# Kernel optimization log

Measured on AMD Instinct MI355X. Metric: run time of the kernel, lower is better.

## Reference

```python
import jax, jax.numpy as jnp
import numpy as np
from jax import lax

N_C = 1024  # number of FPS centroids (hard-coded in forward)
K = 32      # knn neighbors (hard-coded in forward)


def _fps(x, far0):
    # Faithful to the source: dist is recomputed against ONLY the latest
    # centroid each iteration (the mask/min-update in the source is dead code),
    # then far = argmax(dist).
    B = x.shape[0]
    bidx = jnp.arange(B)

    def step(far, _):
        c = x[bidx, far]                              # [B, C]
        d = jnp.sum((x - c[:, None, :]) ** 2, -1)     # [B, N]
        return jnp.argmax(d, -1), c

    _, cents = lax.scan(step, far0, None, length=N_C)  # cents: [n_c, B, C]
    return jnp.transpose(cents, (1, 0, 2))             # [B, n_c, C]


def _knn_group(x, cent):
    # squared euclidean distances (same argsort order as torch.cdist)
    d2 = (jnp.sum(cent ** 2, -1)[..., None]
          + jnp.sum(x ** 2, -1)[:, None, :]
          - 2.0 * jnp.einsum('bmc,bnc->bmn', cent, x))   # [B, n_c, N]
    _, idx = lax.top_k(-d2, K)                            # [B, n_c, K] smallest dists
    neighbors = jax.vmap(lambda xb, ib: xb[ib])(x, idx)   # [B, n_c, K, C]
    return neighbors


def _conv1x1(h, w, b):
    # 1x1 Conv1d == channel matmul; h: [B, Cin, L], w: [Cout, Cin]
    return jax.nn.relu(jnp.einsum('oi,bil->bol', w, h) + b[None, :, None])


def setup_inputs() -> dict:
    key = jax.random.key(0)
    ks = jax.random.split(key, 20)
    B, N, C = 4, 16384, 3
    num_classes = 3
    p = lambda k, shp: (jax.random.normal(k, shp, jnp.float32) * 0.02)
    return {
        'x': jax.random.normal(ks[0], (B, N, C), jnp.float32),
        'far_init': jax.random.randint(ks[1], (B,), 0, N, jnp.int32),
        'w1': p(ks[2], (64, 3)),    'b1': p(ks[3], (64,)),
        'w2': p(ks[4], (64, 64)),   'b2': p(ks[5], (64,)),
        'w3': p(ks[6], (64, 64)),   'b3': p(ks[7], (64,)),
        'w4': p(ks[8], (128, 64)),  'b4': p(ks[9], (128,)),
        'w5': p(ks[10], (1024, 128)), 'b5': p(ks[11], (1024,)),
        'fw1': p(ks[12], (512, 1024)), 'fb1': p(ks[13], (512,)),
        'fw2': p(ks[14], (256, 512)),  'fb2': p(ks[15], (256,)),
        'fw3': p(ks[16], (num_classes, 256)), 'fb3': p(ks[17], (num_classes,)),
    }


def reference(x, far_init, w1, b1, w2, b2, w3, b3, w4, b4, w5, b5,
              fw1, fb1, fw2, fb2, fw3, fb3):
    B, N, C = x.shape
    cent = _fps(x, far_init)                 # [B, n_c, C]
    neighbors = _knn_group(x, cent)          # [B, n_c, K, C]
    h = jnp.transpose(neighbors, (0, 3, 1, 2)).reshape(B, C, N_C * K)
    h = _conv1x1(h, w1, b1)
    h = _conv1x1(h, w2, b2)
    h = _conv1x1(h, w3, b3)
    h = _conv1x1(h, w4, b4)
    h = _conv1x1(h, w5, b5)                  # [B, 1024, n_c*K]
    g = jnp.max(h, axis=2)                   # global max pool -> [B, 1024]
    g = jax.nn.relu(g @ fw1.T + fb1)
    g = jax.nn.relu(g @ fw2.T + fb2)
    return g @ fw3.T + fb3                   # [B, num_classes]
```

## Files before the change

kernel.cpp:

```cpp
#include <hip/hip_runtime.h>

#define BN  4
#define NPT 16384
#define NCC 1024
#define KNN 32

#define HBINS    2048
#define CCH      2
#define CAND_CAP 768

#define OFF_CCOUNT 0
#define OFF_SCOUNT 64
#define OFF_SBITS  128
#define OFF_POOL   (128 + BN*(NPT/32)*4)
#define OFF_CLIST  (OFF_POOL + BN*NCC*4)
#define OFF_H1     (OFF_CLIST + BN*NCC*4)
#define OFF_H2     (OFF_H1 + BN*512*4)
#define OFF_SLIST  (OFF_H2 + BN*256*4)

typedef short bf16x8 __attribute__((ext_vector_type(8)));
typedef float f32x4  __attribute__((ext_vector_type(4)));
typedef float f32x2  __attribute__((ext_vector_type(2)));

__device__ __forceinline__ short f2bf(float f) {
    unsigned u = __float_as_uint(f);
    return (short)((u + 0x7fffu + ((u >> 16) & 1u)) >> 16);
}
__device__ __forceinline__ bf16x8 cvt8(const float* __restrict__ p) {
    bf16x8 v;
#pragma unroll
    for (int j = 0; j < 8; ++j) v[j] = f2bf(p[j]);
    return v;
}

__global__ __launch_bounds__(1024) void fps_kernel(const float* __restrict__ x,
    const int* __restrict__ far_init, int* __restrict__ clist, int* __restrict__ ccount,
    int* __restrict__ scount, unsigned* __restrict__ sbits, float* __restrict__ pool)
{
#pragma clang fp contract(off)
    const int b = blockIdx.x, t = threadIdx.x;
    __shared__ __align__(16) unsigned char seen[NPT];
    __shared__ unsigned long long slot[3];

    if (t < 512) sbits[b*(NPT/32) + t] = 0u;
    pool[b*NCC + t] = 0.0f;
    if (t == 0) { ccount[b] = 0; scount[b] = 0; }

    const float* xb = x + (size_t)b * NPT * 3;
    f32x2 px[8], py[8], pz[8];
#pragma unroll
    for (int r = 0; r < 8; ++r) {
        int ia = t + ((2*r) << 10), ib = ia + 1024;
        px[r] = f32x2{xb[ia*3+0], xb[ib*3+0]};
        py[r] = f32x2{xb[ia*3+1], xb[ib*3+1]};
        pz[r] = f32x2{xb[ia*3+2], xb[ib*3+2]};
    }
    ((uint4*)seen)[t] = make_uint4(0,0,0,0);
    if (t == 0) { slot[0] = 0ull; slot[1] = 0ull; slot[2] = 0ull; }
    int prev_bx = far_init[b];
    __syncthreads();
    int pbs = __builtin_amdgcn_readfirstlane(prev_bx);
    float cx = xb[pbs*3], cy = xb[pbs*3+1], cz = xb[pbs*3+2];

    int done = 0;
    for (int it = 0; it < NCC-1; ++it) {
        const int p = it % 3;
        const f32x2 cX = {cx, cx}, cY = {cy, cy}, cZ = {cz, cz};
        float best = -1.0f; int bi = 0;
#pragma unroll
        for (int r = 0; r < 8; ++r) {
            f32x2 dx = px[r] - cX;
            f32x2 dy = py[r] - cY;
            f32x2 dz = pz[r] - cZ;
            f32x2 m1 = dx * dx;
            f32x2 m2 = dy * dy;
            f32x2 m3 = dz * dz;
            f32x2 s  = (m1 + m2) + m3;
            int ia = t + ((2*r) << 10);
            if (s.x > best) { best = s.x; bi = ia; }
            if (s.y > best) { best = s.y; bi = ia + 1024; }
        }
#pragma unroll
        for (int m = 1; m < 64; m <<= 1) {
            float od = __shfl_xor(best, m, 64);
            int   oi = __shfl_xor(bi,   m, 64);
            if (od > best || (od == best && oi < bi)) { best = od; bi = oi; }
        }
        if ((t & 63) == 0) {
            unsigned long long pk =
                (((unsigned long long)__float_as_uint(best)) << 32)
                | (unsigned)(NPT - 1 - bi);
            atomicMax(&slot[p], pk);
        }
        if (t == 0) seen[prev_bx] = 1;
        __syncthreads();
        int bx = NPT - 1 - (int)(unsigned)(slot[p] & 0xFFFFFFFFull);
        if (t == 0) slot[(it + 2) % 3] = 0ull;
        if (seen[bx]) { done = 1; break; }
        prev_bx = bx;
        int bxs = __builtin_amdgcn_readfirstlane(bx);
        cx = xb[bxs*3]; cy = xb[bxs*3+1]; cz = xb[bxs*3+2];
    }
    if (!done && t == 0) seen[prev_bx] = 1;
    __syncthreads();
#pragma unroll
    for (int j = 0; j < 16; ++j) {
        int idx = t + (j << 10);
        if (seen[idx]) {
            int pos = atomicAdd(&ccount[b], 1);
            clist[b * NCC + pos] = idx;
        }
    }
}

__device__ __forceinline__ unsigned key_of(float px, float py, float pz, float xn,
                                           float cx, float cy, float cz, float cn)
{
    float dot = __fadd_rn(__fadd_rn(__fmul_rn(cx,px), __fmul_rn(cy,py)), __fmul_rn(cz,pz));
    float d2  = __fsub_rn(__fadd_rn(cn, xn), __fmul_rn(2.0f, dot));
    unsigned u = __float_as_uint(d2);
    return u ^ ((u >> 31) ? 0xFFFFFFFFu : 0x80000000u);
}

__device__ __forceinline__ void wave_scan_bins(const unsigned* __restrict__ H,
    int nbins, int rem, int lane, int* __restrict__ out_bin, int* __restrict__ out_below)
{
    int per = nbins >> 6;
    int base = lane * per;
    unsigned part = 0;
    for (int q = 0; q < per; ++q) part += H[base + q];
    unsigned inc = part;
#pragma unroll
    for (int m = 1; m < 64; m <<= 1) {
        unsigned u = __shfl_up(inc, m, 64);
        if (lane >= m) inc += u;
    }
    unsigned exc = inc - part;
    unsigned long long mk = __ballot(exc < (unsigned)rem && inc >= (unsigned)rem);
    int src = __ffsll((long long)mk) - 1;
    if (lane == src) {
        unsigned run = exc; int bb = base;
        for (int q = 0; q < per; ++q) {
            unsigned h = H[base + q];
            if (run + h >= (unsigned)rem) { bb = base + q; break; }
            run += h;
        }
        *out_bin = bb; *out_below = (int)run;
    }
}

__global__ __launch_bounds__(1024) void knn_kernel(const float* __restrict__ x,
    const int* __restrict__ clist, const int* __restrict__ ccount,
    unsigned* __restrict__ sbits, int* __restrict__ slist, int* __restrict__ scount)
{
    const int b = blockIdx.y, t = threadIdx.x;
    const int lane = t & 63, w = t >> 6;
    const int cnt = ccount[b];
    const int cbase = blockIdx.x * CCH;
    if (cbase >= cnt) return;
    const float* xb = x + (size_t)b * NPT * 3;

    __shared__ unsigned hist[CCH * HBINS];
    __shared__ unsigned cand[CCH * CAND_CAP];
    __shared__ float cpx[CCH], cpy[CCH], cpz[CCH], cpn[CCH];
    __shared__ unsigned candCnt[CCH];
    __shared__ int s_bb[CCH], s_below[CCH], s_rrem[CCH], s_need[CCH], s_pref[CCH];
    __shared__ unsigned s_tau[CCH];
    __shared__ int s_tbin, s_tbelow;

    if (t < CCH) {
        int ci = clist[b * NCC + min(cbase + t, cnt - 1)];
        float cx = xb[ci*3], cy = xb[ci*3+1], cz = xb[ci*3+2];
        cpx[t] = cx; cpy[t] = cy; cpz[t] = cz;
        cpn[t] = __fadd_rn(__fadd_rn(__fmul_rn(cx,cx), __fmul_rn(cy,cy)), __fmul_rn(cz,cz));
        candCnt[t] = 0;
    }
    for (int i = t; i < CCH * HBINS; i += 1024) hist[i] = 0;
    __syncthreads();

    unsigned keys[NPT/1024][CCH];
#pragma unroll
    for (int j = 0; j < NPT/1024; ++j) {
        int i = t + (j << 10);
        float px = xb[i*3], py = xb[i*3+1], pz = xb[i*3+2];
        float xn = __fadd_rn(__fadd_rn(__fmul_rn(px,px), __fmul_rn(py,py)), __fmul_rn(pz,pz));
#pragma unroll
        for (int c = 0; c < CCH; ++c) {
            unsigned key = key_of(px,py,pz,xn, cpx[c],cpy[c],cpz[c],cpn[c]);
            keys[j][c] = key;
            atomicAdd(&hist[c*HBINS + (key >> 21)], 1u);
        }
    }
    __syncthreads();

    if (w < CCH)
        wave_scan_bins(&hist[w*HBINS], HBINS, KNN, lane, &s_bb[w], &s_below[w]);
    __syncthreads();
    if (t < CCH) s_rrem[t] = KNN - s_below[t];
    __syncthreads();

#pragma unroll
    for (int j = 0; j < NPT/1024; ++j) {
#pragma unroll
        for (int c = 0; c < CCH; ++c) {
            unsigned key = keys[j][c];
            if ((int)(key >> 21) == s_bb[c]) {
                unsigned pos = atomicAdd(&candCnt[c], 1u);
                if (pos < CAND_CAP) cand[c*CAND_CAP + pos] = key;
            }
        }
    }
    __syncthreads();

    if (w < CCH) {
        unsigned cc = candCnt[w];
        if (cc <= CAND_CAP) {
            int r = s_rrem[w] - 1;
            const unsigned* C = &cand[w*CAND_CAP];
            for (int idx = lane; idx < (int)cc; idx += 64) {
                unsigned k = C[idx]; int rank = 0;
                for (int q = 0; q < (int)cc; ++q) {
                    unsigned kq = C[q];
                    rank += (kq < k || (kq == k && q < idx)) ? 1 : 0;
                }
                if (rank == r) s_tau[w] = k;
            }
            if (lane == 0) s_need[w] = 0;
        } else if (lane == 0) s_need[w] = 1;
    }
    __syncthreads();

    for (int c = 0; c < CCH; ++c) {
        if (s_need[c]) {
            const float cx = cpx[c], cy = cpy[c], cz = cpz[c], cn = cpn[c];
            for (int i = t; i < HBINS; i += 1024) hist[i] = 0;
            __syncthreads();
            for (int j = 0; j < NPT/1024; ++j) {
                int i = t + (j << 10);
                float px = xb[i*3], py = xb[i*3+1], pz = xb[i*3+2];
                float xn = __fadd_rn(__fadd_rn(__fmul_rn(px,px), __fmul_rn(py,py)), __fmul_rn(pz,pz));
                unsigned key = key_of(px,py,pz,xn, cx,cy,cz,cn);
                if ((int)(key >> 21) == s_bb[c]) atomicAdd(&hist[(key >> 10) & 2047u], 1u);
            }
            __syncthreads();
            if (w == 0) wave_scan_bins(hist, HBINS, s_rrem[c], lane, &s_tbin, &s_tbelow);
            __syncthreads();
            if (t == 0) { s_pref[c] = (s_bb[c] << 11) | s_tbin; s_rrem[c] -= s_tbelow; }
            __syncthreads();
            for (int i = t; i < 1024; i += 1024) hist[i] = 0;
            __syncthreads();
            for (int j = 0; j < NPT/1024; ++j) {
                int i = t + (j << 10);
                float px = xb[i*3], py = xb[i*3+1], pz = xb[i*3+2];
                float xn = __fadd_rn(__fadd_rn(__fmul_rn(px,px), __fmul_rn(py,py)), __fmul_rn(pz,pz));
                unsigned key = key_of(px,py,pz,xn, cx,cy,cz,cn);
                if ((int)(key >> 10) == s_pref[c]) atomicAdd(&hist[key & 1023u], 1u);
            }
            __syncthreads();
            if (w == 0) wave_scan_bins(hist, 1024, s_rrem[c], lane, &s_tbin, &s_tbelow);
            __syncthreads();
            if (t == 0) s_tau[c] = (((unsigned)s_pref[c]) << 10) | (unsigned)s_tbin;
            __syncthreads();
        }
    }
    __syncthreads();

#pragma unroll
    for (int j = 0; j < NPT/1024; ++j) {
        int i = t + (j << 10);
        bool sel = false;
#pragma unroll
        for (int c = 0; c < CCH; ++c) sel |= (keys[j][c] <= s_tau[c]);
        if (sel) {
            unsigned bit = 1u << (i & 31);
            unsigned old = atomicOr(&sbits[b*(NPT/32) + (i >> 5)], bit);
            if (!(old & bit)) {
                int pos = atomicAdd(&scount[b], 1);
                slist[b * NPT + pos] = i;
            }
        }
    }
}

#define MFMA16(a, bfr, c) __builtin_amdgcn_mfma_f32_16x16x32_bf16(a, bfr, c, 0, 0, 0)

__global__ __launch_bounds__(1024) void mlp_kernel(const float* __restrict__ x,
    const int* __restrict__ sel_list, const int* __restrict__ sel_count,
    const float* __restrict__ w1, const float* __restrict__ b1,
    const float* __restrict__ w2, const float* __restrict__ b2,
    const float* __restrict__ w3, const float* __restrict__ b3,
    const float* __restrict__ w4, const float* __restrict__ b4,
    const float* __restrict__ w5, const float* __restrict__ b5,
    float* __restrict__ pool)
{
    const int b = blockIdx.y, z = blockIdx.z, t = threadIdx.x;
    const int cnt = sel_count[b];
    if ((blockIdx.x << 6) >= cnt) return;
    const int lane = t & 63;
    const int w    = __builtin_amdgcn_readfirstlane(t >> 6);
    const int m    = lane & 15, quad = lane >> 4;

    __shared__ __align__(16) short A1[64 * 72];
    __shared__ __align__(16) short A2[64 * 72];
    __shared__ __align__(16) short A3[64 * 136];
    __shared__ float sx[3 * 64];

    const int ocA = (w >> 2) * 16 + m;
    bf16x8 bw2[2], bw3[2], bw4[2][2], bw5[4];
#pragma unroll
    for (int ks = 0; ks < 2; ++ks) {
        bw2[ks] = cvt8(w2 + ocA*64 + ks*32 + quad*8);
        bw3[ks] = cvt8(w3 + ocA*64 + ks*32 + quad*8);
    }
    int oc4i[2];
#pragma unroll
    for (int r2 = 0; r2 < 2; ++r2) {
        oc4i[r2] = ((w >> 2) + 4*r2) * 16 + m;
#pragma unroll
        for (int ks = 0; ks < 2; ++ks)
            bw4[r2][ks] = cvt8(w4 + oc4i[r2]*64 + ks*32 + quad*8);
    }
    const int oc5 = z*256 + w*16 + m;
#pragma unroll
    for (int ks = 0; ks < 4; ++ks)
        bw5[ks] = cvt8(w5 + oc5*128 + ks*32 + quad*8);
    const float bias2 = b2[ocA], bias3 = b3[ocA];
    const float bias4_0 = b4[oc4i[0]], bias4_1 = b4[oc4i[1]];
    const float bias5 = b5[oc5];
    float w1v[4][3], b1v[4];
#pragma unroll
    for (int i = 0; i < 4; ++i) {
        int oc = w*4 + i;
        w1v[i][0] = w1[oc*3+0]; w1v[i][1] = w1[oc*3+1]; w1v[i][2] = w1[oc*3+2];
        b1v[i] = b1[oc];
    }
    const int pt0 = (w & 3) * 16;

    for (int base = blockIdx.x << 6; base < cnt; base += (32 << 6)) {
        const int npts = min(64, cnt - base);
        __syncthreads();
        if (t < 64) {
            int idx = sel_list[b * NPT + base + min(t, npts - 1)];
            const float* xp = x + ((size_t)b * NPT + idx) * 3;
            sx[t] = xp[0]; sx[64 + t] = xp[1]; sx[128 + t] = xp[2];
        }
        __syncthreads();
        {
            float x0 = sx[lane], x1 = sx[64 + lane], x2 = sx[128 + lane];
#pragma unroll
            for (int i = 0; i < 4; ++i) {
                float acc = fmaf(x2, w1v[i][2], fmaf(x1, w1v[i][1],
                             fmaf(x0, w1v[i][0], b1v[i])));
                A1[lane*72 + w*4 + i] = f2bf(fmaxf(acc, 0.0f));
            }
        }
        __syncthreads();
        {
            bf16x8 a0 = *(const bf16x8*)&A1[(pt0 + m)*72 + quad*8];
            bf16x8 a1 = *(const bf16x8*)&A1[(pt0 + m)*72 + 32 + quad*8];
            f32x4 d = {0.f, 0.f, 0.f, 0.f};
            d = MFMA16(a0, bw2[0], d);
            d = MFMA16(a1, bw2[1], d);
#pragma unroll
            for (int r = 0; r < 4; ++r)
                A2[(pt0 + quad*4 + r)*72 + ocA] = f2bf(fmaxf(d[r] + bias2, 0.0f));
        }
        __syncthreads();
        {
            bf16x8 a0 = *(const bf16x8*)&A2[(pt0 + m)*72 + quad*8];
            bf16x8 a1 = *(const bf16x8*)&A2[(pt0 + m)*72 + 32 + quad*8];
            f32x4 d = {0.f, 0.f, 0.f, 0.f};
            d = MFMA16(a0, bw3[0], d);
            d = MFMA16(a1, bw3[1], d);
#pragma unroll
            for (int r = 0; r < 4; ++r)
                A1[(pt0 + quad*4 + r)*72 + ocA] = f2bf(fmaxf(d[r] + bias3, 0.0f));
        }
        __syncthreads();
        {
            bf16x8 a0 = *(const bf16x8*)&A1[(pt0 + m)*72 + quad*8];
            bf16x8 a1 = *(const bf16x8*)&A1[(pt0 + m)*72 + 32 + quad*8];
#pragma unroll
            for (int r2 = 0; r2 < 2; ++r2) {
                f32x4 d = {0.f, 0.f, 0.f, 0.f};
                d = MFMA16(a0, bw4[r2][0], d);
                d = MFMA16(a1, bw4[r2][1], d);
                float bs = r2 ? bias4_1 : bias4_0;
#pragma unroll
                for (int r = 0; r < 4; ++r)
                    A3[(pt0 + quad*4 + r)*136 + oc4i[r2]] = f2bf(fmaxf(d[r] + bs, 0.0f));
            }
        }
        __syncthreads();
        {
            float vm = 0.0f;
#pragma unroll
            for (int pt4 = 0; pt4 < 4; ++pt4) {
                const int q0 = pt4 * 16;
                f32x4 d = {0.f, 0.f, 0.f, 0.f};
#pragma unroll
                for (int ks = 0; ks < 4; ++ks) {
                    bf16x8 a = *(const bf16x8*)&A3[(q0 + m)*136 + ks*32 + quad*8];
                    d = MFMA16(a, bw5[ks], d);
                }
#pragma unroll
                for (int r = 0; r < 4; ++r)
                    vm = fmaxf(vm, fmaxf(d[r] + bias5, 0.0f));
            }
            vm = fmaxf(vm, __shfl_xor(vm, 16, 64));
            vm = fmaxf(vm, __shfl_xor(vm, 32, 64));
            if (lane < 16)
                atomicMax((int*)&pool[b*NCC + z*256 + w*16 + lane], __float_as_int(vm));
        }
    }
}

__global__ __launch_bounds__(1024) void head1_kernel(const float* __restrict__ pool,
    const float* __restrict__ fw1, const float* __restrict__ fb1,
    float* __restrict__ h1g)
{
    const int bo = blockIdx.x, b = blockIdx.y, t = threadIdx.x;
    const int lane = t & 63, w = t >> 6;
    __shared__ float g[1024];
    g[t] = pool[b*NCC + t];
    __syncthreads();
#pragma unroll
    for (int i = 0; i < 2; ++i) {
        int o = bo * 32 + w * 2 + i;
        float acc = 0.0f;
#pragma unroll
        for (int j = 0; j < 16; ++j) {
            int k = lane + (j << 6);
            acc += g[k] * fw1[o*1024 + k];
        }
#pragma unroll
        for (int m = 1; m < 64; m <<= 1) acc += __shfl_xor(acc, m, 64);
        if (lane == 0) h1g[b*512 + o] = fmaxf(acc + fb1[o], 0.0f);
    }
}

__global__ __launch_bounds__(1024) void head2_kernel(const float* __restrict__ h1g,
    const float* __restrict__ fw2, const float* __restrict__ fb2,
    float* __restrict__ h2g)
{
    const int bo = blockIdx.x, b = blockIdx.y, t = threadIdx.x;
    const int lane = t & 63, w = t >> 6;
    __shared__ float h1[512];
    if (t < 512) h1[t] = h1g[b*512 + t];
    __syncthreads();
#pragma unroll
    for (int i = 0; i < 2; ++i) {
        int o = bo * 32 + w * 2 + i;
        float acc = 0.0f;
#pragma unroll
        for (int j = 0; j < 8; ++j) {
            int k = lane + (j << 6);
            acc += h1[k] * fw2[o*512 + k];
        }
#pragma unroll
        for (int m = 1; m < 64; m <<= 1) acc += __shfl_xor(acc, m, 64);
        if (lane == 0) h2g[b*256 + o] = fmaxf(acc + fb2[o], 0.0f);
    }
}

__global__ __launch_bounds__(256) void head3_kernel(const float* __restrict__ h2g,
    const float* __restrict__ fw3, const float* __restrict__ fb3,
    float* __restrict__ out)
{
    const int b = blockIdx.x, t = threadIdx.x;
    const int lane = t & 63, w = t >> 6;
    __shared__ float h2[256];
    h2[t] = h2g[b*256 + t];
    __syncthreads();
    if (w < 3) {
        float acc = 0.0f;
#pragma unroll
        for (int j = 0; j < 4; ++j) {
            int k = lane + (j << 6);
            acc += h2[k] * fw3[w*256 + k];
        }
#pragma unroll
        for (int m = 1; m < 64; m <<= 1) acc += __shfl_xor(acc, m, 64);
        if (lane == 0) out[b*3 + w] = acc + fb3[w];
    }
}

extern "C" void kernel_launch(void* const* d_in, const int* in_sizes, int n_in,
                              void* d_out, int out_size, void* d_ws, size_t ws_size,
                              hipStream_t stream)
{
    const float* x    = (const float*)d_in[0];
    const int*   far0 = (const int*)  d_in[1];
    const float *w1 = (const float*)d_in[2],  *b1 = (const float*)d_in[3];
    const float *w2 = (const float*)d_in[4],  *b2 = (const float*)d_in[5];
    const float *w3 = (const float*)d_in[6],  *b3 = (const float*)d_in[7];
    const float *w4 = (const float*)d_in[8],  *b4 = (const float*)d_in[9];
    const float *w5 = (const float*)d_in[10], *b5 = (const float*)d_in[11];
    const float *fw1 = (const float*)d_in[12], *fb1 = (const float*)d_in[13];
    const float *fw2 = (const float*)d_in[14], *fb2 = (const float*)d_in[15];
    const float *fw3 = (const float*)d_in[16], *fb3 = (const float*)d_in[17];

    char* ws = (char*)d_ws;
    int*      ccount = (int*)     (ws + OFF_CCOUNT);
    int*      scount = (int*)     (ws + OFF_SCOUNT);
    unsigned* sbits  = (unsigned*)(ws + OFF_SBITS);
    float*    pool   = (float*)   (ws + OFF_POOL);
    int*      clist  = (int*)     (ws + OFF_CLIST);
    float*    h1g    = (float*)   (ws + OFF_H1);
    float*    h2g    = (float*)   (ws + OFF_H2);
    int*      slist  = (int*)     (ws + OFF_SLIST);

    fps_kernel<<<BN, 1024, 0, stream>>>(x, far0, clist, ccount, scount, sbits, pool);
    knn_kernel<<<dim3(NCC/CCH, BN), 1024, 0, stream>>>(x, clist, ccount, sbits, slist, scount);
    mlp_kernel<<<dim3(32, BN, 4), 1024, 0, stream>>>(x, slist, scount,
        w1,b1, w2,b2, w3,b3, w4,b4, w5,b5, pool);
    head1_kernel<<<dim3(16, BN), 1024, 0, stream>>>(pool, fw1, fb1, h1g);
    head2_kernel<<<dim3(8, BN), 1024, 0, stream>>>(h1g, fw2, fb2, h2g);
    head3_kernel<<<BN, 256, 0, stream>>>(h2g, fw3, fb3, (float*)d_out);
}
```

Baseline: 158.0 us.

## Split FPS argmax into value-max then index resolution, pass centroid coords via LDS

Each FPS iteration now reduces only the float max across the wave, using fmax shuffles instead of paired value/index shuffles. After a barrier, the threads whose local max equals the global max find their smallest matching index, atomicMin it, and publish that point's coordinates through a small LDS slot. This drops the index shuffle work and the global-memory reload of the next centroid on the critical path. In exchange it adds a second __syncthreads per iteration and keeps eight distance pairs live in registers.

```diff
diff --git a/kernel.cpp b/kernel.cpp
--- a/kernel.cpp
+++ b/kernel.cpp
@@ -40,7 +40,10 @@
 #pragma clang fp contract(off)
     const int b = blockIdx.x, t = threadIdx.x;
     __shared__ __align__(16) unsigned char seen[NPT];
-    __shared__ unsigned long long slot[3];
+    __shared__ unsigned vslot[2];
+    __shared__ int      islot[2];
+    __shared__ int      nmatch[2];
+    __shared__ __align__(16) int4 cslot[2][4];
 
     if (t < 512) sbits[b*(NPT/32) + t] = 0u;
     pool[b*NCC + t] = 0.0f;
@@ -56,7 +59,11 @@
         pz[r] = f32x2{xb[ia*3+2], xb[ib*3+2]};
     }
     ((uint4*)seen)[t] = make_uint4(0,0,0,0);
-    if (t == 0) { slot[0] = 0ull; slot[1] = 0ull; slot[2] = 0ull; }
+    if (t == 0) {
+        vslot[0] = 0u;         vslot[1] = 0u;
+        islot[0] = 0x7fffffff; islot[1] = 0x7fffffff;
+        nmatch[0] = 0;         nmatch[1] = 0;
+    }
     int prev_bx = far_init[b];
     __syncthreads();
     int pbs = __builtin_amdgcn_readfirstlane(prev_bx);
@@ -64,9 +71,10 @@
 
     int done = 0;
     for (int it = 0; it < NCC-1; ++it) {
-        const int p = it % 3;
+        const int p = it & 1;
         const f32x2 cX = {cx, cx}, cY = {cy, cy}, cZ = {cz, cz};
-        float best = -1.0f; int bi = 0;
+        f32x2 sv[8];
+        f32x2 rm = {0.0f, 0.0f};
 #pragma unroll
         for (int r = 0; r < 8; ++r) {
             f32x2 dx = px[r] - cX;
@@ -76,30 +84,62 @@
             f32x2 m2 = dy * dy;
             f32x2 m3 = dz * dz;
             f32x2 s  = (m1 + m2) + m3;
-            int ia = t + ((2*r) << 10);
-            if (s.x > best) { best = s.x; bi = ia; }
-            if (s.y > best) { best = s.y; bi = ia + 1024; }
-        }
-#pragma unroll
-        for (int m = 1; m < 64; m <<= 1) {
-            float od = __shfl_xor(best, m, 64);
-            int   oi = __shfl_xor(bi,   m, 64);
-            if (od > best || (od == best && oi < bi)) { best = od; bi = oi; }
-        }
-        if ((t & 63) == 0) {
-            unsigned long long pk =
-                (((unsigned long long)__float_as_uint(best)) << 32)
-                | (unsigned)(NPT - 1 - bi);
-            atomicMax(&slot[p], pk);
-        }
+            sv[r] = s;
+            rm.x = fmaxf(rm.x, s.x);
+            rm.y = fmaxf(rm.y, s.y);
+        }
+        float tm = fmaxf(rm.x, rm.y);
+#pragma unroll
+        for (int m = 1; m < 64; m <<= 1)
+            tm = fmaxf(tm, __shfl_xor(tm, m, 64));
+        if ((t & 63) == 0) atomicMax(&vslot[p], __float_as_uint(tm));
         if (t == 0) seen[prev_bx] = 1;
         __syncthreads();
-        int bx = NPT - 1 - (int)(unsigned)(slot[p] & 0xFFFFFFFFull);
-        if (t == 0) slot[(it + 2) % 3] = 0ull;
+        const unsigned bmax = vslot[p];
+        if (t == 0) {
+            vslot[p^1] = 0u; islot[p^1] = 0x7fffffff; nmatch[p^1] = 0;
+        }
+        if (__float_as_uint(tm) == bmax) {
+            int   myidx = 0x7fffffff;
+            float mx = 0.f, my = 0.f, mz = 0.f;
+#pragma unroll
+            for (int r = 0; r < 8; ++r) {
+                int ia = t + ((2*r) << 10);
+                if (__float_as_uint(sv[r].x) == bmax && ia < myidx)
+                    { myidx = ia;        mx = px[r].x; my = py[r].x; mz = pz[r].x; }
+                if (__float_as_uint(sv[r].y) == bmax && ia + 1024 < myidx)
+                    { myidx = ia + 1024; mx = px[r].y; my = py[r].y; mz = pz[r].y; }
+            }
+            if (myidx != 0x7fffffff) {
+                atomicMin(&islot[p], myidx);
+                int cs = atomicAdd(&nmatch[p], 1);
+                if (cs < 4)
+                    cslot[p][cs] = make_int4(myidx, __float_as_int(mx),
+                                             __float_as_int(my), __float_as_int(mz));
+            }
+        }
+        __syncthreads();
+        const int bx = islot[p];
         if (seen[bx]) { done = 1; break; }
         prev_bx = bx;
-        int bxs = __builtin_amdgcn_readfirstlane(bx);
-        cx = xb[bxs*3]; cy = xb[bxs*3+1]; cz = xb[bxs*3+2];
+        const int nm = nmatch[p] < 4 ? nmatch[p] : 4;
+        bool got = false;
+        float nx = 0.f, ny = 0.f, nz = 0.f;
+#pragma unroll
+        for (int csi = 0; csi < 4; ++csi) {
+            if (csi < nm) {
+                int4 v = cslot[p][csi];
+                if (v.x == bx) {
+                    nx = __int_as_float(v.y); ny = __int_as_float(v.z);
+                    nz = __int_as_float(v.w); got = true;
+                }
+            }
+        }
+        if (got) { cx = nx; cy = ny; cz = nz; }
+        else {
+            int bxs = __builtin_amdgcn_readfirstlane(bx);
+            cx = xb[bxs*3]; cy = xb[bxs*3+1]; cz = xb[bxs*3+2];
+        }
     }
     if (!done && t == 0) seen[prev_bx] = 1;
     __syncthreads();
```

Result: slower. 163.3 us (+3.3%).
